# Kernel tuning notes

Hardware: AMD Instinct MI355X
Metric: run time of the kernel (lower is better)

The kernel has to match this reference:

```python
import jax, jax.numpy as jnp
import numpy as np


def _safe_sqrt(x):
    # cdist-style euclidean distance with grad-safe sqrt at 0
    return jnp.sqrt(jnp.maximum(x, 1e-12))


def setup_inputs() -> dict:
    key = jax.random.key(0)
    k1, k2, k3 = jax.random.split(key, 3)
    B, P, D, C, N = 256, 196, 768, 15, 12544
    return {
        "query_features": jax.random.normal(k1, (B, P, D), dtype=jnp.float32),
        "keys": jax.random.normal(k2, (C, P, D), dtype=jnp.float32),
        "embeddings": jax.random.normal(k3, (N, D), dtype=jnp.float32),
        "num_samples": 196,
    }


def _retrieve_key(query_features, keys):
    # torch.cdist(new_flat.unsqueeze(1), keys_flat.unsqueeze(0)).squeeze(1); min over classes
    B = query_features.shape[0]
    C = keys.shape[0]
    q = query_features.reshape(B, -1)  # [B, P*D]
    k = keys.reshape(C, -1)            # [C, P*D]
    sq = (jnp.sum(q * q, axis=1)[:, None]
          + jnp.sum(k * k, axis=1)[None, :]
          - 2.0 * (q @ k.T))           # [B, C] squared distances via GEMM
    d = _safe_sqrt(sq)
    min_dist = jnp.min(d, axis=1)
    min_idx = jnp.argmin(d, axis=1)
    return min_dist, min_idx


def _fps(embeddings, num_samples):
    # furthest_point_sampling_embeddings: iterative cdist-to-last-centroid,
    # running min of distances, argmax picks next centroid.
    # (torch version seeds with a random index; we use index 0 deterministically)
    N = embeddings.shape[0]
    sqn = jnp.sum(embeddings * embeddings, axis=1)  # [N]

    def step(carry, _):
        dists, last = carry
        c = embeddings[last]                          # [D]
        cur = _safe_sqrt(sqn - 2.0 * (embeddings @ c) + jnp.sum(c * c))
        dists = jnp.minimum(dists, cur)
        nxt = jnp.argmax(dists).astype(jnp.int32)
        return (dists, nxt), nxt

    init = (jnp.full((N,), jnp.inf, dtype=embeddings.dtype), jnp.int32(0))
    _, idxs = jax.lax.scan(step, init, None, length=num_samples - 1)
    idxs = jnp.concatenate([jnp.zeros((1,), dtype=idxs.dtype), idxs])
    return embeddings[idxs]  # [num_samples, D]


def reference(query_features, keys, embeddings, num_samples):
    min_dist, min_idx = _retrieve_key(query_features, keys)
    samples = _fps(embeddings, num_samples)
    return min_dist, min_idx, samples
```

## Files before the change

kernel.cpp:

```cpp
#include <hip/hip_runtime.h>
#include <math.h>

typedef unsigned long long u64;
typedef unsigned int u32;

#define L_TOT  150528
#define ROW4   37632
#define NCHUNK 7
#define CH4    5376
#define R_ITERS 84
#define NBT    32
#define BTILE  8
#define NCLS   15

#define N_E    12544
#define DIM    768
#define NBLK   256
#define PPB    49
#define NSAMP  196
#define EPB    (PPB*DIM)
#define WSTRIDE 16

__device__ __forceinline__ float wave_sum(float v) {
#pragma unroll
  for (int m = 1; m < 64; m <<= 1) v += __shfl_xor(v, m, 64);
  return v;
}

__global__ __launch_bounds__(256) void retrieve_partial(
    const float* __restrict__ q, const float* __restrict__ k,
    float* __restrict__ part, float* __restrict__ kkpart) {
  const int bt = blockIdx.x;
  const int lc = blockIdx.y;
  const int tid = threadIdx.x;
  const int w = tid >> 6, lane = tid & 63;
  const int cbase = w * 4;
  const int ccnt = (w == 3) ? 3 : 4;
  const float4* qf = (const float4*)q;
  const float4* kf = (const float4*)k;
  const int fbase = lc * CH4 + lane;

  float acc[BTILE][4];
  float qq[BTILE];
  float kkv[4];
#pragma unroll
  for (int b = 0; b < BTILE; ++b) {
    qq[b] = 0.f;
#pragma unroll
    for (int c = 0; c < 4; ++c) acc[b][c] = 0.f;
  }
#pragma unroll
  for (int c = 0; c < 4; ++c) kkv[c] = 0.f;

  for (int it = 0; it < R_ITERS; ++it) {
    const int f = fbase + it * 64;
    float4 kv[4];
#pragma unroll
    for (int c = 0; c < 4; ++c)
      if (c < ccnt) kv[c] = kf[(size_t)(cbase + c) * ROW4 + f];
    if (bt == 0) {
#pragma unroll
      for (int c = 0; c < 4; ++c)
        if (c < ccnt)
          kkv[c] += kv[c].x*kv[c].x + kv[c].y*kv[c].y + kv[c].z*kv[c].z + kv[c].w*kv[c].w;
    }
#pragma unroll
    for (int b = 0; b < BTILE; ++b) {
      float4 qv = qf[(size_t)(bt * BTILE + b) * ROW4 + f];
#pragma unroll
      for (int c = 0; c < 4; ++c)
        if (c < ccnt)
          acc[b][c] += qv.x*kv[c].x + qv.y*kv[c].y + qv.z*kv[c].z + qv.w*kv[c].w;
      if (w == 3)
        qq[b] += qv.x*qv.x + qv.y*qv.y + qv.z*qv.z + qv.w*qv.w;
    }
  }

  const size_t pb = (size_t)(lc * NBT + bt) * 16;
#pragma unroll
  for (int b = 0; b < BTILE; ++b) {
#pragma unroll
    for (int c = 0; c < 4; ++c) {
      float v = wave_sum(acc[b][c]);
      if (lane == 0 && c < ccnt) part[(pb + cbase + c) * 8 + b] = v;
    }
    if (w == 3) {
      float v = wave_sum(qq[b]);
      if (lane == 0) part[(pb + 15) * 8 + b] = v;
    }
  }
  if (bt == 0) {
#pragma unroll
    for (int c = 0; c < 4; ++c) {
      float v = wave_sum(kkv[c]);
      if (lane == 0 && c < ccnt) kkpart[lc * 16 + cbase + c] = v;
    }
  }
}

__global__ __launch_bounds__(256) void retrieve_reduce(
    const float* __restrict__ part, const float* __restrict__ kkpart,
    float* __restrict__ out) {
  __shared__ float kn[NCLS];
  const int t = threadIdx.x;
  if (t < NCLS) {
    float s = 0.f;
    for (int lc = 0; lc < NCHUNK; ++lc) s += kkpart[lc * 16 + t];
    kn[t] = s;
  }
  __syncthreads();
  const int bt = t >> 3, bi = t & 7;
  float qq = 0.f;
  for (int lc = 0; lc < NCHUNK; ++lc)
    qq += part[((size_t)(lc * NBT + bt) * 16 + 15) * 8 + bi];
  float dmin = INFINITY;
  int didx = 0;
  for (int c = 0; c < NCLS; ++c) {
    float dot = 0.f;
    for (int lc = 0; lc < NCHUNK; ++lc)
      dot += part[((size_t)(lc * NBT + bt) * 16 + c) * 8 + bi];
    float d2 = qq + kn[c] - 2.f * dot;
    float d = sqrtf(fmaxf(d2, 1e-12f));
    if (d < dmin) { dmin = d; didx = c; }
  }
  out[t] = dmin;
  out[256 + t] = (float)didx;
}

__global__ __launch_bounds__(1024, 4) void fps_kernel(
    const float* __restrict__ emb,
    u64* __restrict__ words,
    float* __restrict__ out_samples) {
  extern __shared__ float e_lds[];
  const int tid = threadIdx.x;
  const int blk = blockIdx.x;
  const int w = tid >> 6, lane = tid & 63;
  const int q4 = lane >> 4;
  const int r = lane & 15;
  const int pl = w * 4 + q4;
  const bool valid = pl < PPB;
  const int p = valid ? pl : 0;

  __shared__ int hist[NSAMP];
  __shared__ u64 wkey[16];
  __shared__ u64 swin[4];

  {
    const float* src = emb + (size_t)blk * EPB;
    for (int i = tid; i < EPB; i += 1024) e_lds[i] = src[i];
  }
  __syncthreads();

  const float4* ef = (const float4*)(e_lds + (size_t)p * DIM);
  float sq;
  {
    float ss = 0.f;
#pragma unroll
    for (int jj = 0; jj < 12; ++jj) {
      float4 v = ef[r + jj * 16];
      ss = fmaf(v.x, v.x, ss); ss = fmaf(v.y, v.y, ss);
      ss = fmaf(v.z, v.z, ss); ss = fmaf(v.w, v.w, ss);
    }
#pragma unroll
    for (int m = 1; m < 16; m <<= 1) ss += __shfl_xor(ss, m, 64);
    sq = ss;
  }
  float dist2 = INFINITY;
  int last = 0;
  if (tid == 0) hist[0] = 0;
  __syncthreads();

  for (int s = 1; s < NSAMP; ++s) {
    const int buf = (s & 1) * NBLK;

    const float4* cf = (const float4*)(emb + (size_t)last * DIM);
    float4 cv[12];
#pragma unroll
    for (int jj = 0; jj < 12; ++jj) cv[jj] = cf[r + jj * 16];

    float a = 0.f, cn = 0.f;
#pragma unroll
    for (int jj = 0; jj < 12; ++jj) {
      float4 e4 = ef[r + jj * 16];
      float4 c4 = cv[jj];
      a = fmaf(e4.x, c4.x, a); a = fmaf(e4.y, c4.y, a);
      a = fmaf(e4.z, c4.z, a); a = fmaf(e4.w, c4.w, a);
      cn = fmaf(c4.x, c4.x, cn); cn = fmaf(c4.y, c4.y, cn);
      cn = fmaf(c4.z, c4.z, cn); cn = fmaf(c4.w, c4.w, cn);
    }
#pragma unroll
    for (int m = 1; m < 16; m <<= 1) {
      a += __shfl_xor(a, m, 64);
      cn += __shfl_xor(cn, m, 64);
    }

    u64 key = 0ull;
    if (valid) {
      float d2 = sq - 2.f * a + cn;
      if (d2 < dist2) dist2 = d2;
      key = ((u64)__float_as_uint(dist2) << 32) |
            (u32)(~(u32)(blk * PPB + pl));
    }
#pragma unroll
    for (int m = 16; m < 64; m <<= 1) {
      u64 o = __shfl_xor(key, m, 64);
      if (o > key) key = o;
    }
    if (lane == 0) wkey[w] = key;
    __syncthreads();

    if (w == 0) {
      u64 k = wkey[lane & 15];
#pragma unroll
      for (int m = 1; m < 16; m <<= 1) {
        u64 o = __shfl_xor(k, m, 64);
        if (o > k) k = o;
      }
      if (lane == 0) {
        const u32 bidx = ~(u32)(k & 0xffffffffull);
        const u32 bdist = (u32)(k >> 32);
        const u64 word = ((u64)s << 48) | ((u64)bdist << 16) | (u64)bidx;
        __hip_atomic_store(&words[(size_t)(buf + blk) * WSTRIDE], word,
                           __ATOMIC_RELAXED, __HIP_MEMORY_SCOPE_AGENT);
      }
    }

    if (tid < NBLK) {
      u64 w64;
      const u64* slot = &words[(size_t)(buf + tid) * WSTRIDE];
      for (;;) {
        w64 = __hip_atomic_load(slot, __ATOMIC_RELAXED,
                                __HIP_MEMORY_SCOPE_AGENT);
        if ((w64 >> 48) >= (u64)s) break;
      }
      u64 kk = (((w64 >> 16) & 0xffffffffull) << 32) |
               (u64)(u32)(~(u32)(w64 & 0xffffull));
#pragma unroll
      for (int m = 1; m < 64; m <<= 1) {
        u64 o = __shfl_xor(kk, m, 64);
        if (o > kk) kk = o;
      }
      if (lane == 0) swin[w] = kk;
    }
    __syncthreads();
    if (tid == 0) {
      u64 m = swin[0];
#pragma unroll
      for (int qi = 1; qi < 4; ++qi) if (swin[qi] > m) m = swin[qi];
      hist[s] = (int)(~(u32)(m & 0xffffffffull));
    }
    __syncthreads();
    last = hist[s];
  }

  if (blk < NSAMP) {
    const int idx = hist[blk];
    const float4* src = (const float4*)(emb + (size_t)idx * DIM);
    float4* dst = (float4*)(out_samples + (size_t)blk * DIM);
    if (tid < DIM / 4) dst[tid] = src[tid];
  }
}

extern "C" void kernel_launch(void* const* d_in, const int* in_sizes, int n_in,
                              void* d_out, int out_size, void* d_ws, size_t ws_size,
                              hipStream_t stream) {
  const float* q   = (const float*)d_in[0];
  const float* k   = (const float*)d_in[1];
  const float* emb = (const float*)d_in[2];
  float* out = (float*)d_out;

  u64* words = (u64*)d_ws;
  float* part   = (float*)((char*)d_ws + 65536);
  float* kkpart = part + 28672;

  hipMemsetAsync(words, 0, 2 * NBLK * WSTRIDE * sizeof(u64), stream);

  hipLaunchKernelGGL(retrieve_partial, dim3(NBT, NCHUNK), dim3(256), 0, stream,
                     q, k, part, kkpart);
  hipLaunchKernelGGL(retrieve_reduce, dim3(1), dim3(256), 0, stream,
                     part, kkpart, out);

  hipFuncSetAttribute((const void*)fps_kernel,
                      hipFuncAttributeMaxDynamicSharedMemorySize,
                      EPB * sizeof(float));

  float* samples = out + 512;
  void* args[] = {(void*)&emb, (void*)&words, (void*)&samples};
  hipLaunchCooperativeKernel((void*)fps_kernel, dim3(NBLK), dim3(1024), args,
                             EPB * sizeof(float), stream);
}
```

Measured before the change: 907.9 us.

## Replace all-to-all FPS grid exchange with hub gather and replicated broadcast

Each farthest-point-sampling step previously had every block poll all 256 per-block candidate words to find the global argmax. Now block 0 alone gathers the candidates, reduces them with LDS atomics, and writes the winner to 8 replicated result slots. The other blocks poll only one of those slots. The per-block reduction also switches from a shared-memory wave-key array plus a barrier to LDS atomicMax with an arrival counter. This is meant to cut global polling traffic and one barrier per step, at the cost of an extra communication hop through the hub block on the serial critical path.

```diff
diff --git a/kernel.cpp b/kernel.cpp
--- a/kernel.cpp
+++ b/kernel.cpp
@@ -19,12 +19,23 @@
 #define PPB    49
 #define NSAMP  196
 #define EPB    (PPB*DIM)
-#define WSTRIDE 16
+#define RSTRIDE 16
 
 __device__ __forceinline__ float wave_sum(float v) {
 #pragma unroll
   for (int m = 1; m < 64; m <<= 1) v += __shfl_xor(v, m, 64);
   return v;
+}
+
+__device__ __forceinline__ u64 key_from_word(u64 w) {
+  return (((w >> 16) & 0xffffffffull) << 32) |
+         (u64)(u32)(~(u32)(w & 0xffffull));
+}
+
+__device__ __forceinline__ u64 word_from_key(u64 s, u64 k) {
+  const u32 bidx = ~(u32)(k & 0xffffffffull);
+  const u32 bdist = (u32)(k >> 32);
+  return (s << 48) | ((u64)bdist << 16) | (u64)bidx;
 }
 
 __global__ __launch_bounds__(256) void retrieve_partial(
@@ -129,7 +140,7 @@
 
 __global__ __launch_bounds__(1024, 4) void fps_kernel(
     const float* __restrict__ emb,
-    u64* __restrict__ words,
+    u64* __restrict__ ws64,
     float* __restrict__ out_samples) {
   extern __shared__ float e_lds[];
   const int tid = threadIdx.x;
@@ -141,13 +152,23 @@
   const bool valid = pl < PPB;
   const int p = valid ? pl : 0;
 
+  u64* hubw = ws64;
+  u64* res8 = ws64 + 512;
+
   __shared__ int hist[NSAMP];
-  __shared__ u64 wkey[16];
-  __shared__ u64 swin[4];
+  __shared__ u64 bkey[2];
+  __shared__ u32 wcnt[2];
+  __shared__ u64 gkey[2];
+  __shared__ u32 gcnt[2];
 
   {
     const float* src = emb + (size_t)blk * EPB;
     for (int i = tid; i < EPB; i += 1024) e_lds[i] = src[i];
+  }
+  if (tid == 0) {
+    hist[0] = 0;
+    bkey[0] = bkey[1] = 0ull;  wcnt[0] = wcnt[1] = 0u;
+    gkey[0] = gkey[1] = 0ull;  gcnt[0] = gcnt[1] = 0u;
   }
   __syncthreads();
 
@@ -167,11 +188,11 @@
   }
   float dist2 = INFINITY;
   int last = 0;
-  if (tid == 0) hist[0] = 0;
   __syncthreads();
 
   for (int s = 1; s < NSAMP; ++s) {
-    const int buf = (s & 1) * NBLK;
+    const int par = s & 1;
+    const int buf = par * NBLK;
 
     const float4* cf = (const float4*)(emb + (size_t)last * DIM);
     float4 cv[12];
@@ -206,50 +227,55 @@
       u64 o = __shfl_xor(key, m, 64);
       if (o > key) key = o;
     }
-    if (lane == 0) wkey[w] = key;
-    __syncthreads();
-
-    if (w == 0) {
-      u64 k = wkey[lane & 15];
-#pragma unroll
-      for (int m = 1; m < 16; m <<= 1) {
-        u64 o = __shfl_xor(k, m, 64);
-        if (o > k) k = o;
-      }
-      if (lane == 0) {
-        const u32 bidx = ~(u32)(k & 0xffffffffull);
-        const u32 bdist = (u32)(k >> 32);
-        const u64 word = ((u64)s << 48) | ((u64)bdist << 16) | (u64)bidx;
-        __hip_atomic_store(&words[(size_t)(buf + blk) * WSTRIDE], word,
+
+    if (lane == 0) {
+      atomicMax(&bkey[par], key);
+      u32 prev = atomicAdd(&wcnt[par], 1u);
+      if (prev == 15u) {
+        u64 k = atomicMax(&bkey[par], 0ull);
+        __hip_atomic_store(&hubw[buf + blk], word_from_key((u64)s, k),
                            __ATOMIC_RELAXED, __HIP_MEMORY_SCOPE_AGENT);
       }
     }
 
-    if (tid < NBLK) {
-      u64 w64;
-      const u64* slot = &words[(size_t)(buf + tid) * WSTRIDE];
-      for (;;) {
-        w64 = __hip_atomic_load(slot, __ATOMIC_RELAXED,
-                                __HIP_MEMORY_SCOPE_AGENT);
-        if ((w64 >> 48) >= (u64)s) break;
+    if (blk == 0) {
+      if (tid < NBLK) {
+        u64 w64;
+        for (;;) {
+          w64 = __hip_atomic_load(&hubw[buf + tid], __ATOMIC_RELAXED,
+                                  __HIP_MEMORY_SCOPE_AGENT);
+          if ((w64 >> 48) >= (u64)s) break;
+        }
+        atomicMax(&gkey[par], key_from_word(w64));
+        u32 gp = atomicAdd(&gcnt[par], 1u);
+        if (gp == (u32)(NBLK - 1)) {
+          u64 m = atomicMax(&gkey[par], 0ull);
+          const int widx = (int)(~(u32)(m & 0xffffffffull));
+          const u64 rw = ((u64)s << 32) | (u32)widx;
+#pragma unroll
+          for (int c = 0; c < 8; ++c)
+            __hip_atomic_store(&res8[(size_t)c * RSTRIDE], rw,
+                               __ATOMIC_RELAXED, __HIP_MEMORY_SCOPE_AGENT);
+          hist[s] = widx;
+          bkey[par] = 0ull; wcnt[par] = 0u;
+          gkey[par] = 0ull; gcnt[par] = 0u;
+        }
       }
-      u64 kk = (((w64 >> 16) & 0xffffffffull) << 32) |
-               (u64)(u32)(~(u32)(w64 & 0xffffull));
-#pragma unroll
-      for (int m = 1; m < 64; m <<= 1) {
-        u64 o = __shfl_xor(kk, m, 64);
-        if (o > kk) kk = o;
+      __syncthreads();
+    } else {
+      if (tid == 0) {
+        const u64* rp = &res8[(size_t)(blk & 7) * RSTRIDE];
+        u64 rr;
+        for (;;) {
+          rr = __hip_atomic_load(rp, __ATOMIC_RELAXED,
+                                 __HIP_MEMORY_SCOPE_AGENT);
+          if ((rr >> 32) >= (u64)s) break;
+        }
+        hist[s] = (int)(u32)(rr & 0xffffffffull);
+        bkey[par] = 0ull; wcnt[par] = 0u;
       }
-      if (lane == 0) swin[w] = kk;
-    }
-    __syncthreads();
-    if (tid == 0) {
-      u64 m = swin[0];
-#pragma unroll
-      for (int qi = 1; qi < 4; ++qi) if (swin[qi] > m) m = swin[qi];
-      hist[s] = (int)(~(u32)(m & 0xffffffffull));
-    }
-    __syncthreads();
+      __syncthreads();
+    }
     last = hist[s];
   }
 
@@ -269,11 +295,11 @@
   const float* emb = (const float*)d_in[2];
   float* out = (float*)d_out;
 
-  u64* words = (u64*)d_ws;
-  float* part   = (float*)((char*)d_ws + 65536);
+  u64* ws64 = (u64*)d_ws;
+  float* part   = (float*)((char*)d_ws + 8192);
   float* kkpart = part + 28672;
 
-  hipMemsetAsync(words, 0, 2 * NBLK * WSTRIDE * sizeof(u64), stream);
+  hipMemsetAsync(d_ws, 0, 8192, stream);
 
   hipLaunchKernelGGL(retrieve_partial, dim3(NBT, NCHUNK), dim3(256), 0, stream,
                      q, k, part, kkpart);
@@ -285,7 +311,7 @@
                       EPB * sizeof(float));
 
   float* samples = out + 512;
-  void* args[] = {(void*)&emb, (void*)&words, (void*)&samples};
+  void* args[] = {(void*)&emb, (void*)&ws64, (void*)&samples};
   hipLaunchCooperativeKernel((void*)fps_kernel, dim3(NBLK), dim3(1024), args,
                              EPB * sizeof(float), stream);
 }
```

Result: slower. 1.449 ms (+59.6%).
